# Performance work log

Hardware: AMD Instinct MI355X
Metric: run time of the kernel (lower is better)

## Reference

```python
import jax, jax.numpy as jnp
import numpy as np

D_IN = 1024
D_OUT = 1024
NUM_HEADS = 16
HEAD_DIM = D_OUT // NUM_HEADS


def setup_inputs() -> dict:
    key = jax.random.key(0)
    ks = jax.random.split(key, 6)
    s = 0.02
    x = jax.random.normal(ks[0], (1, 4096, D_IN), dtype=jnp.float32)
    W_q = jax.random.normal(ks[1], (D_IN, D_OUT), dtype=jnp.float32) * s
    W_k = jax.random.normal(ks[2], (D_IN, D_OUT), dtype=jnp.float32) * s
    W_v = jax.random.normal(ks[3], (D_IN, D_OUT), dtype=jnp.float32) * s
    W_o = jax.random.normal(ks[4], (D_OUT, D_OUT), dtype=jnp.float32) * s
    b_o = jnp.zeros((D_OUT,), dtype=jnp.float32)
    return {"x": x, "W_q": W_q, "W_k": W_k, "W_v": W_v, "W_o": W_o, "b_o": b_o}


def reference(x, W_q, W_k, W_v, W_o, b_o):
    b, n, _ = x.shape
    # project and split heads: [b, h, n, d]
    def split_heads(t):
        return t.reshape(b, n, NUM_HEADS, HEAD_DIM).transpose(0, 2, 1, 3)
    q = split_heads(x @ W_q)
    k = split_heads(x @ W_k)
    v = split_heads(x @ W_v)
    scale = 1.0 / jnp.sqrt(jnp.float32(HEAD_DIM))
    scores = jnp.einsum('bhqd,bhkd->bhqk', q, k) * scale  # [b,h,n,n]
    causal = jnp.tril(jnp.ones((n, n), dtype=bool))
    scores = jnp.where(causal, scores, -jnp.inf)
    weights = jax.nn.softmax(scores, axis=-1)
    # dropout rate is 0.0 -> identity
    ctx = jnp.einsum('bhqk,bhkd->bhqd', weights, v)
    ctx = ctx.transpose(0, 2, 1, 3).reshape(b, n, D_OUT)
    return ctx @ W_o + b_o
```

## Files before the change

### kernel.cpp

```cpp
#include <hip/hip_runtime.h>
#include <hip/hip_bf16.h>

typedef __hip_bfloat16 bf16;
typedef __attribute__((ext_vector_type(8))) short short8;
typedef __attribute__((ext_vector_type(4))) float floatx4;

#define SEQ 4096
#define DIM 1024
#define NH 16
#define HD 64

#if defined(__has_builtin)
#if __has_builtin(__builtin_amdgcn_exp2f)
#define EXP2(x) __builtin_amdgcn_exp2f(x)
#endif
#endif
#ifndef EXP2
#define EXP2(x) exp2f(x)
#endif

__device__ __forceinline__ short f2s(float f) { bf16 t = __float2bfloat16(f); return *(short*)&t; }

__device__ __forceinline__ void gload16(const void* g, void* l) {
    __builtin_amdgcn_global_load_lds(
        (const __attribute__((address_space(1))) void*)g,
        (__attribute__((address_space(3))) void*)l, 16, 0, 0);
}

__device__ __forceinline__ void barrier_lgkm() {
    asm volatile("s_waitcnt lgkmcnt(0)" ::: "memory");
    __builtin_amdgcn_s_barrier();
}

__device__ __forceinline__ short8 cvt8(float4 a, float4 b) {
    short8 s;
    s[0] = f2s(a.x); s[1] = f2s(a.y); s[2] = f2s(a.z); s[3] = f2s(a.w);
    s[4] = f2s(b.x); s[5] = f2s(b.y); s[6] = f2s(b.z); s[7] = f2s(b.w);
    return s;
}

__global__ __launch_bounds__(256) void transpose_cast_kernel(
    const float* __restrict__ W0, const float* __restrict__ W1,
    const float* __restrict__ W2, const float* __restrict__ W3,
    bf16* __restrict__ Wt_all)
{
    const float* W = blockIdx.z == 0 ? W0 : blockIdx.z == 1 ? W1
                   : blockIdx.z == 2 ? W2 : W3;
    bf16* Wt = Wt_all + (size_t)blockIdx.z * DIM * DIM;

    __shared__ float tile[32][33];
    const int n0 = blockIdx.x * 32, k0 = blockIdx.y * 32;
    const int tr = threadIdx.x >> 5;
    const int tc = threadIdx.x & 31;
#pragma unroll
    for (int i = 0; i < 32; i += 8)
        tile[tr + i][tc] = W[(size_t)(k0 + tr + i) * DIM + n0 + tc];
    __syncthreads();
#pragma unroll
    for (int i = 0; i < 32; i += 8)
        Wt[(size_t)(n0 + tr + i) * DIM + k0 + tc] = __float2bfloat16(tile[tc][tr + i]);
}

#define QBM 128
#define QBN 128
#define QBK 64

__global__ __launch_bounds__(256) void qkv_gemm_kernel(
    const float* __restrict__ A, const bf16* __restrict__ Wt,
    bf16* __restrict__ Qb, bf16* __restrict__ Kb, bf16* __restrict__ Vb)
{
    const int z = blockIdx.z;
    const bf16* Bt = Wt + (size_t)z * DIM * DIM;
    bf16* C = z == 0 ? Qb : (z == 1 ? Kb : Vb);
    const float osc = (z == 0) ? 0.18033688f : 1.0f;

    __shared__ alignas(16) float Af[QBM][QBK];
    __shared__ alignas(16) short Bs[QBN][QBK];

    const int tid  = threadIdx.x;
    const int wave = tid >> 6, lane = tid & 63;
    const int l15  = lane & 15, quad = lane >> 4;
    const int wm = (wave & 1) * 64;
    const int wn = (wave >> 1) * 64;
    const int bm = blockIdx.y * QBM;
    const int bn = blockIdx.x * QBN;

    const int arow = tid >> 4;
    const int agch = (tid & 15) ^ (arow & 15);
    const float* gA = A + (size_t)(bm + arow) * DIM + agch * 4;
    char* ldsA = (char*)&Af[0][0] + wave * 1024;

    const int brow = tid >> 3;
    const int bgch = (tid & 7) ^ (brow & 7);
    const bf16* gB = Bt + (size_t)(bn + brow) * DIM + bgch * 8;
    char* ldsB = (char*)&Bs[0][0] + wave * 1024;

    floatx4 acc[4][4] = {};

    for (int k0 = 0; k0 < DIM; k0 += QBK) {
        __syncthreads();
#pragma unroll
        for (int c = 0; c < 8; ++c)
            gload16(gA + (size_t)c * 16 * DIM + k0, ldsA + c * 4096);
#pragma unroll
        for (int c = 0; c < 4; ++c)
            gload16(gB + (size_t)c * 32 * DIM + k0, ldsB + c * 4096);
        __syncthreads();

#pragma unroll
        for (int c2 = 0; c2 < 2; ++c2) {
            const int g0 = c2 * 8 + quad * 2;
            const int cb = (c2 * 4 + quad) ^ (l15 & 7);
            short8 afr[4], bfr[4];
#pragma unroll
            for (int i = 0; i < 4; ++i) {
                const int ra = wm + i * 16 + l15;
                float4 f0 = *(const float4*)&Af[ra][(g0 ^ l15) * 4];
                float4 f1 = *(const float4*)&Af[ra][((g0 + 1) ^ l15) * 4];
                afr[i] = cvt8(f0, f1);
                bfr[i] = *(const short8*)&Bs[wn + i * 16 + l15][cb * 8];
            }
#pragma unroll
            for (int mi = 0; mi < 4; ++mi)
#pragma unroll
                for (int ni = 0; ni < 4; ++ni)
                    acc[mi][ni] = __builtin_amdgcn_mfma_f32_16x16x32_bf16(
                        afr[mi], bfr[ni], acc[mi][ni], 0, 0, 0);
        }
    }

#pragma unroll
    for (int mi = 0; mi < 4; ++mi)
#pragma unroll
        for (int r = 0; r < 4; ++r) {
            const int row = bm + wm + mi * 16 + quad * 4 + r;
#pragma unroll
            for (int ni = 0; ni < 4; ++ni) {
                const int col = bn + wn + ni * 16 + l15;
                C[(size_t)row * DIM + col] = __float2bfloat16(acc[mi][ni][r] * osc);
            }
        }
}

__global__ __launch_bounds__(256) void out_gemm_kernel(
    const bf16* __restrict__ A, const bf16* __restrict__ Bt,
    const float* __restrict__ bias, float* __restrict__ C)
{
    __shared__ alignas(16) short Asl[128][64];
    __shared__ alignas(16) short Bsl[64][64];

    const int tid  = threadIdx.x;
    const int wave = tid >> 6, lane = tid & 63;
    const int l15  = lane & 15, quad = lane >> 4;
    const int wm = (wave & 1) * 64;
    const int wn = (wave >> 1) * 32;
    const int bm = blockIdx.y * 128;
    const int bn = blockIdx.x * 64;

    const int srow   = tid >> 3;
    const int gchunk = (tid & 7) ^ (srow & 7);
    const bf16* gA = A  + (size_t)(bm + srow) * DIM + gchunk * 8;
    const bf16* gB = Bt + (size_t)(bn + srow) * DIM + gchunk * 8;
    char* ldsA = (char*)&Asl[0][0] + wave * 1024;
    char* ldsB = (char*)&Bsl[0][0] + wave * 1024;

    floatx4 acc[4][2] = {};

    for (int k0 = 0; k0 < DIM; k0 += 64) {
        __syncthreads();
#pragma unroll
        for (int c = 0; c < 4; ++c)
            gload16(gA + (size_t)c * 32 * DIM + k0, ldsA + c * 4096);
#pragma unroll
        for (int c = 0; c < 2; ++c)
            gload16(gB + (size_t)c * 32 * DIM + k0, ldsB + c * 4096);
        __syncthreads();

#pragma unroll
        for (int c2 = 0; c2 < 2; ++c2) {
            const int cb = (c2 * 4 + quad) ^ (l15 & 7);
            short8 afr[4], bfr[2];
#pragma unroll
            for (int i = 0; i < 4; ++i)
                afr[i] = *(const short8*)&Asl[wm + i * 16 + l15][cb * 8];
#pragma unroll
            for (int i = 0; i < 2; ++i)
                bfr[i] = *(const short8*)&Bsl[wn + i * 16 + l15][cb * 8];
#pragma unroll
            for (int mi = 0; mi < 4; ++mi)
#pragma unroll
                for (int ni = 0; ni < 2; ++ni)
                    acc[mi][ni] = __builtin_amdgcn_mfma_f32_16x16x32_bf16(
                        afr[mi], bfr[ni], acc[mi][ni], 0, 0, 0);
        }
    }

#pragma unroll
    for (int mi = 0; mi < 4; ++mi)
#pragma unroll
        for (int r = 0; r < 4; ++r) {
            const int row = bm + wm + mi * 16 + quad * 4 + r;
#pragma unroll
            for (int ni = 0; ni < 2; ++ni) {
                const int col = bn + wn + ni * 16 + l15;
                C[(size_t)row * DIM + col] = acc[mi][ni][r] + bias[col];
            }
        }
}

#define QT 128
#define KT 64
#define LDT 72

__global__ __launch_bounds__(512) void flash_attn_kernel(
    const bf16* __restrict__ Q, const bf16* __restrict__ K,
    const bf16* __restrict__ V, bf16* ctx)
{
    const int lin  = blockIdx.y * 32 + blockIdx.x;
    const int half = lin >> 8, idx = lin & 255;
    const int qj   = half ? (idx & 31) : 31 - (idx & 31);
    const int h    = (idx >> 5) + 8 * half;
    const int q0   = qj * QT;
    const int nkt  = 2 * qj + 2;

    const int tid  = threadIdx.x;
    const int wave = tid >> 6;
    const int lane = tid & 63;
    const int l15  = lane & 15;
    const int quad = lane >> 4;

    __shared__ alignas(16) short Ks[2][KT][LDT];
    __shared__ alignas(16) short Vt[2][HD][LDT];

    short8 qfrag[2];
    {
        const bf16* qp = Q + (size_t)(q0 + wave * 16 + l15) * DIM
                       + h * HD + quad * 8;
        qfrag[0] = *(const short8*)(qp);
        qfrag[1] = *(const short8*)(qp + 32);
    }

    const int kr = tid >> 3, kc = (tid & 7) * 8;
    const bool vstager = tid < 256;
    const int vr = (tid & 31) * 2, vd = ((tid >> 5) & 7) * 8;
    const int vslot = ((vr >> 5) & 1) * 32 + ((vr >> 2) & 3) * 8
                    + ((vr >> 4) & 1) * 4  + ((vr >> 1) & 1) * 2;

    short8 kreg, vreg0, vreg1;
    kreg = *(const short8*)(K + (size_t)kr * DIM + h * HD + kc);
    if (vstager) {
        vreg0 = *(const short8*)(V + (size_t)vr * DIM + h * HD + vd);
        vreg1 = *(const short8*)(V + (size_t)(vr + 1) * DIM + h * HD + vd);
    }
    *(short8*)&Ks[0][kr][kc] = kreg;
    if (vstager) {
#pragma unroll
        for (int i = 0; i < 8; ++i) {
            unsigned int pv = (unsigned int)(unsigned short)vreg0[i]
                            | ((unsigned int)(unsigned short)vreg1[i] << 16);
            *(unsigned int*)&Vt[0][vd + i][vslot] = pv;
        }
    }
    kreg = *(const short8*)(K + (size_t)(KT + kr) * DIM + h * HD + kc);
    if (vstager) {
        vreg0 = *(const short8*)(V + (size_t)(KT + vr) * DIM + h * HD + vd);
        vreg1 = *(const short8*)(V + (size_t)(KT + vr + 1) * DIM + h * HD + vd);
    }

    barrier_lgkm();

    short8 onesf;
#pragma unroll
    for (int i = 0; i < 8; ++i) onesf[i] = (short)0x3F80;

    floatx4 o_acc[4] = {};
    floatx4 lacc = {};

    for (int kt = 0; kt < nkt; ++kt) {
        const int b = kt & 1;

        floatx4 sT[4] = {};
#pragma unroll
        for (int n = 0; n < 4; ++n)
#pragma unroll
            for (int c = 0; c < 2; ++c) {
                short8 kf = *(const short8*)&Ks[b][n * 16 + l15][c * 32 + quad * 8];
                sT[n] = __builtin_amdgcn_mfma_f32_16x16x32_bf16(
                    kf, qfrag[c], sT[n], 0, 0, 0);
            }

        if (kt + 1 < nkt) {
            *(short8*)&Ks[b ^ 1][kr][kc] = kreg;
            if (vstager) {
#pragma unroll
                for (int i = 0; i < 8; ++i) {
                    unsigned int pv = (unsigned int)(unsigned short)vreg0[i]
                                    | ((unsigned int)(unsigned short)vreg1[i] << 16);
                    *(unsigned int*)&Vt[b ^ 1][vd + i][vslot] = pv;
                }
            }
            if (kt + 2 < nkt) {
                const size_t nb = (size_t)(kt + 2) * KT;
                kreg = *(const short8*)(K + (nb + kr) * DIM + h * HD + kc);
                if (vstager) {
                    vreg0 = *(const short8*)(V + (nb + vr) * DIM + h * HD + vd);
                    vreg1 = *(const short8*)(V + (nb + vr + 1) * DIM + h * HD + vd);
                }
            }
        }

        short8 pfrag[2];
        const int kbase = kt * KT;
        if (kt >= nkt - 2) {
            const int qrow = q0 + wave * 16 + l15;
            float p[4][4];
#pragma unroll
            for (int n = 0; n < 4; ++n) {
                const int key0 = kbase + n * 16 + quad * 4;
#pragma unroll
                for (int r = 0; r < 4; ++r)
                    p[n][r] = (key0 + r <= qrow) ? EXP2(sT[n][r]) : 0.f;
            }
#pragma unroll
            for (int c = 0; c < 2; ++c) {
                short8 f;
#pragma unroll
                for (int j = 0; j < 8; ++j)
                    f[j] = f2s(p[c * 2 + (j >> 2)][j & 3]);
                pfrag[c] = f;
            }
        } else {
#pragma unroll
            for (int c = 0; c < 2; ++c) {
                short8 f;
#pragma unroll
                for (int j = 0; j < 8; ++j)
                    f[j] = f2s(EXP2(sT[c * 2 + (j >> 2)][j & 3]));
                pfrag[c] = f;
            }
        }

#pragma unroll
        for (int n = 0; n < 4; ++n)
#pragma unroll
            for (int c = 0; c < 2; ++c) {
                short8 vf = *(const short8*)&Vt[b][n * 16 + l15][c * 32 + quad * 8];
                o_acc[n] = __builtin_amdgcn_mfma_f32_16x16x32_bf16(
                    pfrag[c], vf, o_acc[n], 0, 0, 0);
            }
        lacc = __builtin_amdgcn_mfma_f32_16x16x32_bf16(pfrag[0], onesf, lacc, 0, 0, 0);
        lacc = __builtin_amdgcn_mfma_f32_16x16x32_bf16(pfrag[1], onesf, lacc, 0, 0, 0);

        barrier_lgkm();
    }

#pragma unroll
    for (int r = 0; r < 4; ++r) {
        const float inv = 1.0f / lacc[r];
        const int row = q0 + wave * 16 + quad * 4 + r;
#pragma unroll
        for (int n = 0; n < 4; ++n)
            ctx[(size_t)row * DIM + h * HD + n * 16 + l15] =
                __float2bfloat16(o_acc[n][r] * inv);
    }
}

extern "C" void kernel_launch(void* const* d_in, const int* in_sizes, int n_in,
                              void* d_out, int out_size, void* d_ws, size_t ws_size,
                              hipStream_t stream)
{
    const float* x  = (const float*)d_in[0];
    const float* Wq = (const float*)d_in[1];
    const float* Wk = (const float*)d_in[2];
    const float* Wv = (const float*)d_in[3];
    const float* Wo = (const float*)d_in[4];
    const float* bo = (const float*)d_in[5];
    float* out = (float*)d_out;

    bf16* Wt_all = (bf16*)d_ws;
    bf16* Qb     = Wt_all + (size_t)4 * DIM * DIM;
    bf16* V      = (bf16*)d_out;
    bf16* Kb     = V + (size_t)SEQ * DIM;
    bf16* ctx    = Qb;
    const bf16* Wot = Wt_all + (size_t)3 * DIM * DIM;

    transpose_cast_kernel<<<dim3(32, 32, 4), 256, 0, stream>>>(Wq, Wk, Wv, Wo, Wt_all);

    qkv_gemm_kernel<<<dim3(DIM / QBN, SEQ / QBM, 3), 256, 0, stream>>>(
        x, Wt_all, Qb, Kb, V);

    flash_attn_kernel<<<dim3(32, NH), 512, 0, stream>>>(Qb, Kb, V, ctx);

    out_gemm_kernel<<<dim3(DIM / 64, SEQ / 128), 256, 0, stream>>>(
        ctx, Wot, bo, out);
}
```

Before: 190.6 us.

## Split attention key tile across wave pairs with shared-memory reduction of partials

After: 184.3 us. -3.3%, faster.

```diff
diff --git a/kernel.cpp b/kernel.cpp
--- a/kernel.cpp
+++ b/kernel.cpp
@@ -212,7 +212,7 @@
 #define KT 64
 #define LDT 72
 
-__global__ __launch_bounds__(512) void flash_attn_kernel(
+__global__ __launch_bounds__(512, 4) void flash_attn_kernel(
     const bf16* __restrict__ Q, const bf16* __restrict__ K,
     const bf16* __restrict__ V, bf16* ctx)
 {
@@ -225,26 +225,32 @@
 
     const int tid  = threadIdx.x;
     const int wave = tid >> 6;
+    const int qg   = wave & 3;
+    const int kh   = wave >> 2;
     const int lane = tid & 63;
     const int l15  = lane & 15;
     const int quad = lane >> 4;
 
-    __shared__ alignas(16) short Ks[2][KT][LDT];
-    __shared__ alignas(16) short Vt[2][HD][LDT];
-
-    short8 qfrag[2];
-    {
-        const bf16* qp = Q + (size_t)(q0 + wave * 16 + l15) * DIM
+    __shared__ alignas(16) char smem[36864];
+    short (*Ks)[KT][LDT] = (short (*)[KT][LDT])smem;
+    short (*Vt)[HD][LDT] = (short (*)[HD][LDT])(smem + 18432);
+    float* redO = (float*)smem;
+    float* redL = (float*)(smem + 32768);
+
+    short8 qfrag[2][2];
+#pragma unroll
+    for (int s = 0; s < 2; ++s) {
+        const bf16* qp = Q + (size_t)(q0 + qg * 32 + s * 16 + l15) * DIM
                        + h * HD + quad * 8;
-        qfrag[0] = *(const short8*)(qp);
-        qfrag[1] = *(const short8*)(qp + 32);
+        qfrag[s][0] = *(const short8*)(qp);
+        qfrag[s][1] = *(const short8*)(qp + 32);
     }
 
     const int kr = tid >> 3, kc = (tid & 7) * 8;
     const bool vstager = tid < 256;
     const int vr = (tid & 31) * 2, vd = ((tid >> 5) & 7) * 8;
-    const int vslot = ((vr >> 5) & 1) * 32 + ((vr >> 2) & 3) * 8
-                    + ((vr >> 4) & 1) * 4  + ((vr >> 1) & 1) * 2;
+    const int vcol = (vr & 32) + ((vr >> 2) & 3) * 8
+                   + ((vr >> 4) & 1) * 4 + (vr & 3);
 
     short8 kreg, vreg0, vreg1;
     kreg = *(const short8*)(K + (size_t)kr * DIM + h * HD + kc);
@@ -258,7 +264,7 @@
         for (int i = 0; i < 8; ++i) {
             unsigned int pv = (unsigned int)(unsigned short)vreg0[i]
                             | ((unsigned int)(unsigned short)vreg1[i] << 16);
-            *(unsigned int*)&Vt[0][vd + i][vslot] = pv;
+            *(unsigned int*)&Vt[0][vd + i][vcol] = pv;
         }
     }
     kreg = *(const short8*)(K + (size_t)(KT + kr) * DIM + h * HD + kc);
@@ -273,20 +279,23 @@
 #pragma unroll
     for (int i = 0; i < 8; ++i) onesf[i] = (short)0x3F80;
 
-    floatx4 o_acc[4] = {};
-    floatx4 lacc = {};
+    floatx4 o_acc[2][4] = {};
+    floatx4 lacc[2] = {};
 
     for (int kt = 0; kt < nkt; ++kt) {
         const int b = kt & 1;
 
-        floatx4 sT[4] = {};
-#pragma unroll
-        for (int n = 0; n < 4; ++n)
+        floatx4 sT[2][2] = {};
+#pragma unroll
+        for (int n = 0; n < 2; ++n)
 #pragma unroll
             for (int c = 0; c < 2; ++c) {
-                short8 kf = *(const short8*)&Ks[b][n * 16 + l15][c * 32 + quad * 8];
-                sT[n] = __builtin_amdgcn_mfma_f32_16x16x32_bf16(
-                    kf, qfrag[c], sT[n], 0, 0, 0);
+                short8 kf = *(const short8*)
+                    &Ks[b][kh * 32 + n * 16 + l15][c * 32 + quad * 8];
+#pragma unroll
+                for (int s = 0; s < 2; ++s)
+                    sT[s][n] = __builtin_amdgcn_mfma_f32_16x16x32_bf16(
+                        kf, qfrag[s][c], sT[s][n], 0, 0, 0);
             }
 
         if (kt + 1 < nkt) {
@@ -296,7 +305,7 @@
                 for (int i = 0; i < 8; ++i) {
                     unsigned int pv = (unsigned int)(unsigned short)vreg0[i]
                                     | ((unsigned int)(unsigned short)vreg1[i] << 16);
-                    *(unsigned int*)&Vt[b ^ 1][vd + i][vslot] = pv;
+                    *(unsigned int*)&Vt[b ^ 1][vd + i][vcol] = pv;
                 }
             }
             if (kt + 2 < nkt) {
@@ -310,58 +319,88 @@
         }
 
         short8 pfrag[2];
-        const int kbase = kt * KT;
+        const int kbase = kt * KT + kh * 32;
         if (kt >= nkt - 2) {
-            const int qrow = q0 + wave * 16 + l15;
-            float p[4][4];
-#pragma unroll
-            for (int n = 0; n < 4; ++n) {
-                const int key0 = kbase + n * 16 + quad * 4;
+#pragma unroll
+            for (int s = 0; s < 2; ++s) {
+                const int qrow = q0 + qg * 32 + s * 16 + l15;
+                float p[2][4];
+#pragma unroll
+                for (int n = 0; n < 2; ++n) {
+                    const int key0 = kbase + n * 16 + quad * 4;
+#pragma unroll
+                    for (int r = 0; r < 4; ++r)
+                        p[n][r] = (key0 + r <= qrow) ? EXP2(sT[s][n][r]) : 0.f;
+                }
+                short8 f;
+#pragma unroll
+                for (int j = 0; j < 8; ++j)
+                    f[j] = f2s(p[j >> 2][j & 3]);
+                pfrag[s] = f;
+            }
+        } else {
+#pragma unroll
+            for (int s = 0; s < 2; ++s) {
+                short8 f;
+#pragma unroll
+                for (int j = 0; j < 8; ++j)
+                    f[j] = f2s(EXP2(sT[s][j >> 2][j & 3]));
+                pfrag[s] = f;
+            }
+        }
+
+#pragma unroll
+        for (int n = 0; n < 4; ++n) {
+            short8 vf = *(const short8*)
+                &Vt[b][n * 16 + l15][kh * 32 + quad * 8];
+#pragma unroll
+            for (int s = 0; s < 2; ++s)
+                o_acc[s][n] = __builtin_amdgcn_mfma_f32_16x16x32_bf16(
+                    pfrag[s], vf, o_acc[s][n], 0, 0, 0);
+        }
+#pragma unroll
+        for (int s = 0; s < 2; ++s)
+            lacc[s] = __builtin_amdgcn_mfma_f32_16x16x32_bf16(
+                pfrag[s], onesf, lacc[s], 0, 0, 0);
+
+        barrier_lgkm();
+    }
+
+    if (kh == 1) {
+#pragma unroll
+        for (int s = 0; s < 2; ++s)
+#pragma unroll
+            for (int n = 0; n < 4; ++n)
 #pragma unroll
                 for (int r = 0; r < 4; ++r)
-                    p[n][r] = (key0 + r <= qrow) ? EXP2(sT[n][r]) : 0.f;
-            }
-#pragma unroll
-            for (int c = 0; c < 2; ++c) {
-                short8 f;
-#pragma unroll
-                for (int j = 0; j < 8; ++j)
-                    f[j] = f2s(p[c * 2 + (j >> 2)][j & 3]);
-                pfrag[c] = f;
-            }
-        } else {
-#pragma unroll
-            for (int c = 0; c < 2; ++c) {
-                short8 f;
-#pragma unroll
-                for (int j = 0; j < 8; ++j)
-                    f[j] = f2s(EXP2(sT[c * 2 + (j >> 2)][j & 3]));
-                pfrag[c] = f;
-            }
-        }
-
-#pragma unroll
-        for (int n = 0; n < 4; ++n)
-#pragma unroll
-            for (int c = 0; c < 2; ++c) {
-                short8 vf = *(const short8*)&Vt[b][n * 16 + l15][c * 32 + quad * 8];
-                o_acc[n] = __builtin_amdgcn_mfma_f32_16x16x32_bf16(
-                    pfrag[c], vf, o_acc[n], 0, 0, 0);
-            }
-        lacc = __builtin_amdgcn_mfma_f32_16x16x32_bf16(pfrag[0], onesf, lacc, 0, 0, 0);
-        lacc = __builtin_amdgcn_mfma_f32_16x16x32_bf16(pfrag[1], onesf, lacc, 0, 0, 0);
-
-        barrier_lgkm();
-    }
-
-#pragma unroll
-    for (int r = 0; r < 4; ++r) {
-        const float inv = 1.0f / lacc[r];
-        const int row = q0 + wave * 16 + quad * 4 + r;
-#pragma unroll
-        for (int n = 0; n < 4; ++n)
-            ctx[(size_t)row * DIM + h * HD + n * 16 + l15] =
-                __float2bfloat16(o_acc[n][r] * inv);
+                    redO[(size_t)(qg * 32 + s * 16 + quad * 4 + r) * 64
+                         + n * 16 + l15] = o_acc[s][n][r];
+        if (l15 == 0) {
+#pragma unroll
+            for (int s = 0; s < 2; ++s)
+#pragma unroll
+                for (int r = 0; r < 4; ++r)
+                    redL[qg * 32 + s * 16 + quad * 4 + r] = lacc[s][r];
+        }
+    }
+    __syncthreads();
+    if (kh == 0) {
+#pragma unroll
+        for (int s = 0; s < 2; ++s)
+#pragma unroll
+            for (int r = 0; r < 4; ++r) {
+                const int row_l = qg * 32 + s * 16 + quad * 4 + r;
+                const float lsum = lacc[s][r] + redL[row_l];
+                const float inv = 1.0f / lsum;
+                const int row = q0 + row_l;
+#pragma unroll
+                for (int n = 0; n < 4; ++n) {
+                    const float o = o_acc[s][n][r]
+                                  + redO[(size_t)row_l * 64 + n * 16 + l15];
+                    ctx[(size_t)row * DIM + h * HD + n * 16 + l15] =
+                        __float2bfloat16(o * inv);
+                }
+            }
     }
 }
 
```
